# Kernel optimization log

Hardware: AMD Instinct MI355X
Metric: run time of the kernel (lower is better)

Reference implementation:

```python
import jax, jax.numpy as jnp
import numpy as np

N = 100000       # nodes
F_IN = 1433      # input features (Cora)
HID = 67         # hidden dim (hardcoded in module)
C = 7            # classes (Cora)
E = 3200000      # edges (avg degree 32)


def setup_inputs() -> dict:
    key = jax.random.key(0)
    k = jax.random.split(key, 4)
    x = jax.random.normal(k[0], (N, F_IN), dtype=jnp.float32)
    edge_index = jax.random.randint(k[1], (2, E), 0, N, dtype=jnp.int32)
    W1 = jax.random.normal(k[2], (F_IN, HID), dtype=jnp.float32) / np.float32(np.sqrt(F_IN))
    b1 = jnp.zeros((HID,), dtype=jnp.float32)
    W2 = jax.random.normal(k[3], (HID, C), dtype=jnp.float32) / np.float32(np.sqrt(HID))
    b2 = jnp.zeros((C,), dtype=jnp.float32)
    return {"x": x, "edge_index": edge_index, "W1": W1, "b1": b1, "W2": W2, "b2": b2}


def gcn_conv(x, edge_index, W, b):
    """PyG GCNConv: h = W x; out = D^-1/2 (A + I) D^-1/2 h + b."""
    n = x.shape[0]
    h = x @ W  # [n, out_dim]
    loops = jnp.arange(n, dtype=edge_index.dtype)
    row = jnp.concatenate([edge_index[0], loops])  # source
    col = jnp.concatenate([edge_index[1], loops])  # target
    deg = jax.ops.segment_sum(jnp.ones_like(col, dtype=h.dtype), col, num_segments=n)
    dinv = jnp.where(deg > 0, jax.lax.rsqrt(deg), jnp.float32(0))
    norm = dinv[row] * dinv[col]                    # [E+n]
    msg = h[row] * norm[:, None]                    # gather + scale
    out = jax.ops.segment_sum(msg, col, num_segments=n)  # scatter-add
    return out + b


def reference(x, edge_index, W1, b1, W2, b2):
    h = gcn_conv(x, edge_index, W1, b1)
    h = jax.nn.leaky_relu(h, negative_slope=0.01)
    # F.dropout(p=0.951, training=self.training) -> identity in eval mode
    h = gcn_conv(h, edge_index, W2, b2)
    return jax.nn.log_softmax(h, axis=1)
```

## Files before the change

### kernel.cpp

```cpp
#include <hip/hip_runtime.h>
#include <math.h>

#define FIN  1433
#define HID  67
#define NC   7
#define NCP  8

#define BK     32
#define KTILES 45
#define KPAD   (KTILES*BK)
#define COLP   80

typedef __attribute__((ext_vector_type(8))) short short8;
typedef __attribute__((ext_vector_type(4))) float floatx4;

static __device__ inline unsigned short f2bf(float f) {
    unsigned int u = __float_as_uint(f);
    unsigned int r = (u + 0x7fffu + ((u >> 16) & 1u)) >> 16;
    return (unsigned short)r;
}


__global__ void k_zero(int* __restrict__ cnt, int N) {
    int i = blockIdx.x * 256 + threadIdx.x;
    if (i < N) cnt[i] = 0;
}

__global__ void k_count(const int* __restrict__ dst, int* __restrict__ cnt, int E) {
    int e = blockIdx.x * 256 + threadIdx.x;
    if (e < E) atomicAdd(&cnt[dst[e]], 1);
}

__global__ void k_bsum(const int* __restrict__ cnt, int* __restrict__ bsum, int N) {
    __shared__ int s[256];
    int t = threadIdx.x;
    int i = blockIdx.x * 256 + t;
    s[t] = (i < N) ? cnt[i] : 0;
    __syncthreads();
    for (int o = 128; o > 0; o >>= 1) {
        if (t < o) s[t] += s[t + o];
        __syncthreads();
    }
    if (t == 0) bsum[blockIdx.x] = s[0];
}

__global__ void k_scanb(int* __restrict__ bsum, int nb) {
    __shared__ int s[512];
    int t = threadIdx.x;
    int v = (t < nb) ? bsum[t] : 0;
    s[t] = v;
    __syncthreads();
    for (int o = 1; o < 512; o <<= 1) {
        int tmp = (t >= o) ? s[t - o] : 0;
        __syncthreads();
        s[t] += tmp;
        __syncthreads();
    }
    if (t < nb) bsum[t] = s[t] - v;
}

__global__ void k_scan3(const int* __restrict__ cnt, const int* __restrict__ bsum,
                        int* __restrict__ rowptr, int* __restrict__ cursor,
                        float* __restrict__ dinv, int N, int E) {
    __shared__ int s[256];
    int t = threadIdx.x;
    int i = blockIdx.x * 256 + t;
    int v = (i < N) ? cnt[i] : 0;
    s[t] = v;
    __syncthreads();
    for (int o = 1; o < 256; o <<= 1) {
        int tmp = (t >= o) ? s[t - o] : 0;
        __syncthreads();
        s[t] += tmp;
        __syncthreads();
    }
    if (i < N) {
        int start = bsum[blockIdx.x] + s[t] - v;
        rowptr[i] = start;
        cursor[i] = start;
        dinv[i]   = rsqrtf((float)(v + 1));
    }
    if (i == 0) rowptr[N] = E;
}

__global__ void k_fill(const int* __restrict__ ei, int* __restrict__ cursor,
                       int* __restrict__ csrs, int E) {
    int e = blockIdx.x * 256 + threadIdx.x;
    if (e < E) {
        int s = ei[e];
        int d = ei[E + e];
        int pos = atomicAdd(&cursor[d], 1);
        csrs[pos] = s;
    }
}


__global__ void k_wcvt(const float* __restrict__ W1, const float* __restrict__ x,
                       unsigned short* __restrict__ Wt, float* __restrict__ xpad, int N) {
    int idx = blockIdx.x * 256 + threadIdx.x;
    if (idx < KPAD) xpad[idx] = (idx < FIN) ? x[(N - 1) * FIN + idx] : 0.f;
    if (idx >= COLP * KPAD) return;
    int col = idx / KPAD;
    int k   = idx - col * KPAD;
    float v = (col < HID && k < FIN) ? W1[k * HID + col] : 0.f;
    Wt[idx] = f2bf(v);
}


#define GEMM1_LOAD(Abuf, KT) __builtin_memcpy(&Abuf[0], xp0 + (KT), 32)

#define GEMM1_STEP(Abuf, KT) do {                                                   \
        short8 fa;                                                                  \
        _Pragma("unroll")                                                           \
        for (int u = 0; u < 8; u++) fa[u] = (short)f2bf(Abuf[u]);                   \
        _Pragma("unroll")                                                           \
        for (int j = 0; j < 5; j++) {                                               \
            short8 bf = *(const short8*)(wb + j * 16 * KPAD + (KT));                \
            acc[j] = __builtin_amdgcn_mfma_f32_16x16x32_bf16(fa, bf, acc[j], 0, 0, 0); \
        }                                                                           \
    } while (0)

__global__ __launch_bounds__(256) void k_gemm1(const float* __restrict__ x,
                                               const unsigned short* __restrict__ Wt,
                                               const float* __restrict__ dinv,
                                               const float* __restrict__ xpad,
                                               float* __restrict__ h64,
                                               float* __restrict__ h4, int N) {
    int t    = threadIdx.x;
    int lane = t & 63;
    int w    = t >> 6;
    int lm   = lane & 15;
    int lq   = lane >> 4;
    int row0w = blockIdx.x * 64 + w * 16;

    int r0 = row0w + lm;
    const float* xp0 = (r0 >= N - 1) ? xpad : (x + r0 * FIN);
    xp0 += lq * 8;
    const unsigned short* wb = Wt + lm * KPAD + lq * 8;

    floatx4 acc[5];
#pragma unroll
    for (int j = 0; j < 5; j++) acc[j] = (floatx4){0.f, 0.f, 0.f, 0.f};

    float A0[8], A1[8];
    GEMM1_LOAD(A0, 0);
    int kt = 0;
    for (; kt + 2 * BK < KPAD; kt += 2 * BK) {
        GEMM1_LOAD(A1, kt + BK);
        GEMM1_STEP(A0, kt);
        GEMM1_LOAD(A0, kt + 2 * BK);
        GEMM1_STEP(A1, kt + BK);
    }
    GEMM1_STEP(A0, kt);

#pragma unroll
    for (int i = 0; i < 4; i++) {
        int row = row0w + lq * 4 + i;
        if (row < N) {
            float dv = dinv[row];
            int off = row * 64;
#pragma unroll
            for (int j = 0; j < 4; j++) h64[off + j * 16 + lm] = dv * acc[j][i];
            if (lm < 4) h4[row * 4 + lm] = dv * acc[4][i];
        }
    }
}


__global__ __launch_bounds__(256) void k_agg1(const float* __restrict__ h64,
                                              const float* __restrict__ h4,
                                              const int* __restrict__ rowptr,
                                              const int* __restrict__ csrs,
                                              const float* __restrict__ dinv,
                                              const float* __restrict__ bias1,
                                              const float* __restrict__ W2,
                                              float* __restrict__ h2s, int N) {
    int lane = threadIdx.x & 63;
    int d = blockIdx.x * 4 + (threadIdx.x >> 6);
    if (d >= N) return;
    int start = rowptr[d];
    int end   = rowptr[d + 1];
    int tc = lane & 3;

    float m0 = 0.f, m1 = 0.f, m2 = 0.f, m3 = 0.f;
    float t0 = 0.f, t1 = 0.f, t2 = 0.f, t3 = 0.f;
    int e = start;
    for (; e + 4 <= end; e += 4) {
        int s0 = csrs[e], s1 = csrs[e + 1], s2 = csrs[e + 2], s3 = csrs[e + 3];
        m0 += h64[s0 * 64 + lane];  t0 += h4[s0 * 4 + tc];
        m1 += h64[s1 * 64 + lane];  t1 += h4[s1 * 4 + tc];
        m2 += h64[s2 * 64 + lane];  t2 += h4[s2 * 4 + tc];
        m3 += h64[s3 * 64 + lane];  t3 += h4[s3 * 4 + tc];
    }
    for (; e < end; e++) {
        int s = csrs[e];
        m0 += h64[s * 64 + lane];
        t0 += h4[s * 4 + tc];
    }
    float dd = dinv[d];
    float sa = ((m0 + m1) + (m2 + m3)) + h64[d * 64 + lane];
    float sb = ((t0 + t1) + (t2 + t3)) + h4[d * 4 + tc];

    float vm = bias1[lane] + dd * sa;
    vm = vm > 0.f ? vm : 0.01f * vm;
    int tcol = 64 + tc;
    float bb = (tcol < HID) ? bias1[tcol] : 0.f;
    float vt = bb + dd * sb;
    vt = vt > 0.f ? vt : 0.01f * vt;

    float pj[NC];
#pragma unroll
    for (int j = 0; j < NC; j++) {
        float wm = W2[lane * NC + j];
        float wt = (lane < 3) ? W2[(64 + lane) * NC + j] : 0.f;
        pj[j] = vm * wm + vt * wt;
    }
#pragma unroll
    for (int o = 32; o >= 1; o >>= 1) {
#pragma unroll
        for (int j = 0; j < NC; j++) pj[j] += __shfl_xor(pj[j], o);
    }
    if (lane == 0) {
        int off = d * NCP;
#pragma unroll
        for (int j = 0; j < NC; j++) h2s[off + j] = dd * pj[j];
        h2s[off + NC] = 0.f;
    }
}


__global__ __launch_bounds__(256) void k_agg2(const float* __restrict__ h2s,
                                              const int* __restrict__ rowptr,
                                              const int* __restrict__ csrs,
                                              const float* __restrict__ dinv,
                                              const float* __restrict__ b2,
                                              float* __restrict__ out, int N) {
    int lane = threadIdx.x & 63;
    int d = blockIdx.x * 4 + (threadIdx.x >> 6);
    if (d >= N) return;
    int es = lane >> 3;
    int j  = lane & 7;
    int start = rowptr[d], end = rowptr[d + 1];
    float acc = 0.f;
    for (int e = start + es; e < end; e += 8) {
        int s = csrs[e];
        acc += h2s[s * NCP + j];
    }
#pragma unroll
    for (int o = 32; o >= 8; o >>= 1) acc += __shfl_xor(acc, o);
    float dd = dinv[d];
    float self = h2s[d * NCP + j];
    float v = ((j < NC) ? b2[j] : 0.f) + dd * (self + acc);
    float mv = (j == NC) ? -1e30f : v;
#pragma unroll
    for (int o = 4; o >= 1; o >>= 1) mv = fmaxf(mv, __shfl_xor(mv, o));
    float ex = (j == NC) ? 0.f : __expf(v - mv);
    float ss = ex;
#pragma unroll
    for (int o = 4; o >= 1; o >>= 1) ss += __shfl_xor(ss, o);
    if (lane < 8 && j < NC) {
        out[d * NC + j] = v - mv - __logf(ss);
    }
}


extern "C" void kernel_launch(void* const* d_in, const int* in_sizes, int n_in,
                              void* d_out, int out_size, void* d_ws, size_t ws_size,
                              hipStream_t stream) {
    const float* x  = (const float*)d_in[0];
    const int*   ei = (const int*)d_in[1];
    const float* W1 = (const float*)d_in[2];
    const float* b1 = (const float*)d_in[3];
    const float* W2 = (const float*)d_in[4];
    const float* b2 = (const float*)d_in[5];
    float* out = (float*)d_out;

    int N = in_sizes[0] / FIN;
    int E = in_sizes[1] / 2;

    size_t o = 0;
    auto alloc = [&](size_t words) { size_t r = o; o += words; o = (o + 63) & ~(size_t)63; return r; };
    size_t o_dinv   = alloc((size_t)N);
    size_t o_cnt    = alloc((size_t)N);
    size_t o_rowptr = alloc((size_t)N + 1);
    size_t o_cursor = alloc((size_t)N);
    size_t o_bsum   = alloc(1024);
    size_t o_csrs   = alloc((size_t)E);
    size_t o_wt     = alloc((size_t)COLP * KPAD / 2);
    size_t o_xpad   = alloc((size_t)KPAD);
    size_t o_h64    = alloc((size_t)N * 64);
    size_t o_h4     = alloc((size_t)N * 4);
    size_t o_h2s    = alloc((size_t)N * NCP);

    float* wsf = (float*)d_ws;
    int*   wsi = (int*)d_ws;
    float* dinv   = wsf + o_dinv;
    int*   cnt    = wsi + o_cnt;
    int*   rowptr = wsi + o_rowptr;
    int*   cursor = wsi + o_cursor;
    int*   bsum   = wsi + o_bsum;
    int*   csrs   = wsi + o_csrs;
    unsigned short* Wt = (unsigned short*)(wsi + o_wt);
    float* xpad   = wsf + o_xpad;
    float* h64    = wsf + o_h64;
    float* h4     = wsf + o_h4;
    float* h2s    = wsf + o_h2s;

    int nb = (N + 255) / 256;
    int eb = (E + 255) / 256;
    int gb = (N + 63) / 64;

    k_zero <<<nb, 256, 0, stream>>>(cnt, N);
    k_count<<<eb, 256, 0, stream>>>(ei + E, cnt, E);
    k_bsum <<<nb, 256, 0, stream>>>(cnt, bsum, N);
    k_scanb<<<1, 512, 0, stream>>>(bsum, nb);
    k_scan3<<<nb, 256, 0, stream>>>(cnt, bsum, rowptr, cursor, dinv, N, E);
    k_fill <<<eb, 256, 0, stream>>>(ei, cursor, csrs, E);

    k_wcvt <<<(COLP * KPAD + 255) / 256, 256, 0, stream>>>(W1, x, Wt, xpad, N);
    k_gemm1<<<gb, 256, 0, stream>>>(x, Wt, dinv, xpad, h64, h4, N);
    k_agg1 <<<(N + 3) / 4, 256, 0, stream>>>(h64, h4, rowptr, csrs, dinv, b1, W2, h2s, N);
    k_agg2 <<<(N + 3) / 4, 256, 0, stream>>>(h2s, rowptr, csrs, dinv, b2, out, N);
}
```

Baseline: 1.466 ms.

## Build CSR via two-level bucket sort instead of global atomics

Replaces per-edge global atomic counting and filling of the CSR with a two-pass bucketed radix sort. Edges are first binned into 512-node coarse buckets using shared-memory histograms and block-level offsets. Each bucket is then sorted locally in LDS to produce rowptr, csrs and dinv. This cuts contended global atomics and scattered writes, at the cost of an extra E-sized buffer and packed encodings that assume node ids fit in 18 bits and at most 512 coarse buckets.

```diff
diff --git a/kernel.cpp b/kernel.cpp
--- a/kernel.cpp
+++ b/kernel.cpp
@@ -11,6 +11,9 @@
 #define KPAD   (KTILES*BK)
 #define COLP   80
 
+#define CB_BITS 9
+#define CB_SIZE 512
+
 typedef __attribute__((ext_vector_type(8))) short short8;
 typedef __attribute__((ext_vector_type(4))) float floatx4;
 
@@ -21,89 +24,138 @@
 }
 
 
-__global__ void k_zero(int* __restrict__ cnt, int N) {
-    int i = blockIdx.x * 256 + threadIdx.x;
-    if (i < N) cnt[i] = 0;
-}
-
-__global__ void k_count(const int* __restrict__ dst, int* __restrict__ cnt, int E) {
-    int e = blockIdx.x * 256 + threadIdx.x;
-    if (e < E) atomicAdd(&cnt[dst[e]], 1);
-}
-
-__global__ void k_bsum(const int* __restrict__ cnt, int* __restrict__ bsum, int N) {
-    __shared__ int s[256];
-    int t = threadIdx.x;
-    int i = blockIdx.x * 256 + t;
-    s[t] = (i < N) ? cnt[i] : 0;
-    __syncthreads();
-    for (int o = 128; o > 0; o >>= 1) {
-        if (t < o) s[t] += s[t + o];
-        __syncthreads();
-    }
-    if (t == 0) bsum[blockIdx.x] = s[0];
-}
-
-__global__ void k_scanb(int* __restrict__ bsum, int nb) {
-    __shared__ int s[512];
-    int t = threadIdx.x;
-    int v = (t < nb) ? bsum[t] : 0;
-    s[t] = v;
-    __syncthreads();
-    for (int o = 1; o < 512; o <<= 1) {
-        int tmp = (t >= o) ? s[t - o] : 0;
-        __syncthreads();
-        s[t] += tmp;
-        __syncthreads();
-    }
-    if (t < nb) bsum[t] = s[t] - v;
-}
-
-__global__ void k_scan3(const int* __restrict__ cnt, const int* __restrict__ bsum,
-                        int* __restrict__ rowptr, int* __restrict__ cursor,
-                        float* __restrict__ dinv, int N, int E) {
-    __shared__ int s[256];
-    int t = threadIdx.x;
-    int i = blockIdx.x * 256 + t;
-    int v = (i < N) ? cnt[i] : 0;
-    s[t] = v;
-    __syncthreads();
-    for (int o = 1; o < 256; o <<= 1) {
-        int tmp = (t >= o) ? s[t - o] : 0;
-        __syncthreads();
-        s[t] += tmp;
-        __syncthreads();
-    }
-    if (i < N) {
-        int start = bsum[blockIdx.x] + s[t] - v;
-        rowptr[i] = start;
-        cursor[i] = start;
-        dinv[i]   = rsqrtf((float)(v + 1));
-    }
-    if (i == 0) rowptr[N] = E;
-}
-
-__global__ void k_fill(const int* __restrict__ ei, int* __restrict__ cursor,
-                       int* __restrict__ csrs, int E) {
-    int e = blockIdx.x * 256 + threadIdx.x;
-    if (e < E) {
-        int s = ei[e];
-        int d = ei[E + e];
-        int pos = atomicAdd(&cursor[d], 1);
-        csrs[pos] = s;
-    }
-}
-
-
 __global__ void k_wcvt(const float* __restrict__ W1, const float* __restrict__ x,
-                       unsigned short* __restrict__ Wt, float* __restrict__ xpad, int N) {
+                       unsigned short* __restrict__ Wt, float* __restrict__ xpad,
+                       int* __restrict__ gcnt, int N) {
     int idx = blockIdx.x * 256 + threadIdx.x;
+    if (idx < 512) gcnt[idx] = 0;
     if (idx < KPAD) xpad[idx] = (idx < FIN) ? x[(N - 1) * FIN + idx] : 0.f;
     if (idx >= COLP * KPAD) return;
     int col = idx / KPAD;
     int k   = idx - col * KPAD;
     float v = (col < HID && k < FIN) ? W1[k * HID + col] : 0.f;
     Wt[idx] = f2bf(v);
+}
+
+
+__global__ __launch_bounds__(256) void k_cb_count(const int* __restrict__ dst,
+                                                  int* __restrict__ gcnt, int E) {
+    __shared__ int lh[512];
+    int t = threadIdx.x;
+    lh[t] = 0; lh[t + 256] = 0;
+    __syncthreads();
+    int base = blockIdx.x * 4096;
+    for (int i = t; i < 4096; i += 256) {
+        int e = base + i;
+        if (e < E) atomicAdd(&lh[dst[e] >> CB_BITS], 1);
+    }
+    __syncthreads();
+    int v0 = lh[t];       if (v0) atomicAdd(&gcnt[t], v0);
+    int v1 = lh[t + 256]; if (v1) atomicAdd(&gcnt[t + 256], v1);
+}
+
+__global__ void k_cb_scan(const int* __restrict__ gcnt, int* __restrict__ cbase,
+                          int* __restrict__ gcur, int E) {
+    __shared__ int s[512];
+    int t = threadIdx.x;
+    int v = gcnt[t];
+    s[t] = v;
+    __syncthreads();
+    for (int o = 1; o < 512; o <<= 1) {
+        int tmp = (t >= o) ? s[t - o] : 0;
+        __syncthreads();
+        s[t] += tmp;
+        __syncthreads();
+    }
+    int ex = s[t] - v;
+    cbase[t] = ex;
+    gcur[t]  = ex;
+    if (t == 511) cbase[512] = E;
+}
+
+__global__ __launch_bounds__(256) void k_cb_scat(const int* __restrict__ ei,
+                                                 int* __restrict__ gcur,
+                                                 unsigned int* __restrict__ gbuf, int E) {
+    __shared__ int lh[512];
+    __shared__ int gb[512];
+    int t = threadIdx.x;
+    lh[t] = 0; lh[t + 256] = 0;
+    __syncthreads();
+    int base = blockIdx.x * 4096;
+    unsigned int rk[16];
+    unsigned int pk[16];
+#pragma unroll
+    for (int i = 0; i < 16; i++) {
+        int e = base + i * 256 + t;
+        rk[i] = 0xFFFFFFFFu;
+        if (e < E) {
+            int s = ei[e];
+            int d = ei[E + e];
+            int cb = d >> CB_BITS;
+            int r = atomicAdd(&lh[cb], 1);
+            rk[i] = (unsigned int)((cb << 16) | r);
+            pk[i] = (unsigned int)s | ((unsigned int)(d & (CB_SIZE - 1)) << 18);
+        }
+    }
+    __syncthreads();
+    int v0 = lh[t];       gb[t]       = v0 ? atomicAdd(&gcur[t], v0) : 0;
+    int v1 = lh[t + 256]; gb[t + 256] = v1 ? atomicAdd(&gcur[t + 256], v1) : 0;
+    __syncthreads();
+#pragma unroll
+    for (int i = 0; i < 16; i++) {
+        if (rk[i] != 0xFFFFFFFFu) {
+            int cb = rk[i] >> 16, r = rk[i] & 0xFFFF;
+            gbuf[gb[cb] + r] = pk[i];
+        }
+    }
+}
+
+__global__ __launch_bounds__(256) void k_cb_build(const unsigned int* __restrict__ gbuf,
+                                                  const int* __restrict__ cbase,
+                                                  int* __restrict__ rowptr,
+                                                  int* __restrict__ csrs,
+                                                  float* __restrict__ dinv, int N, int E) {
+    __shared__ int hist[512];
+    __shared__ int sc[512];
+    int b = blockIdx.x;
+    int t = threadIdx.x;
+    int n0 = cbase[b], n1 = cbase[b + 1];
+    hist[t] = 0; hist[t + 256] = 0;
+    __syncthreads();
+    for (int i = n0 + t; i < n1; i += 256)
+        atomicAdd(&hist[gbuf[i] >> 18], 1);
+    __syncthreads();
+    sc[t] = hist[t]; sc[t + 256] = hist[t + 256];
+    __syncthreads();
+    for (int o = 1; o < 512; o <<= 1) {
+        int a0 = (t       >= o) ? sc[t - o]       : 0;
+        int a1 = (t + 256 >= o) ? sc[t + 256 - o] : 0;
+        __syncthreads();
+        sc[t] += a0; sc[t + 256] += a1;
+        __syncthreads();
+    }
+#pragma unroll
+    for (int hh = 0; hh < 2; hh++) {
+        int f = t + hh * 256;
+        int d = (b << CB_BITS) + f;
+        int cnt = hist[f];
+        int ex  = sc[f] - cnt;
+        if (d < N) {
+            rowptr[d] = n0 + ex;
+            dinv[d]   = rsqrtf((float)(cnt + 1));
+        }
+    }
+    if (b == 0 && t == 0) rowptr[N] = E;
+    __syncthreads();
+    hist[t]       = sc[t] - hist[t];
+    hist[t + 256] = sc[t + 256] - hist[t + 256];
+    __syncthreads();
+    for (int i = n0 + t; i < n1; i += 256) {
+        unsigned int pkd = gbuf[i];
+        int f = pkd >> 18;
+        int p = atomicAdd(&hist[f], 1);
+        csrs[n0 + p] = (int)(pkd & 0x3FFFFu);
+    }
 }
 
 
@@ -281,11 +333,12 @@
     size_t o = 0;
     auto alloc = [&](size_t words) { size_t r = o; o += words; o = (o + 63) & ~(size_t)63; return r; };
     size_t o_dinv   = alloc((size_t)N);
-    size_t o_cnt    = alloc((size_t)N);
     size_t o_rowptr = alloc((size_t)N + 1);
-    size_t o_cursor = alloc((size_t)N);
-    size_t o_bsum   = alloc(1024);
     size_t o_csrs   = alloc((size_t)E);
+    size_t o_gbuf   = alloc((size_t)E);
+    size_t o_gcnt   = alloc(512);
+    size_t o_cbase  = alloc(513);
+    size_t o_gcur   = alloc(512);
     size_t o_wt     = alloc((size_t)COLP * KPAD / 2);
     size_t o_xpad   = alloc((size_t)KPAD);
     size_t o_h64    = alloc((size_t)N * 64);
@@ -295,29 +348,28 @@
     float* wsf = (float*)d_ws;
     int*   wsi = (int*)d_ws;
     float* dinv   = wsf + o_dinv;
-    int*   cnt    = wsi + o_cnt;
     int*   rowptr = wsi + o_rowptr;
-    int*   cursor = wsi + o_cursor;
-    int*   bsum   = wsi + o_bsum;
     int*   csrs   = wsi + o_csrs;
+    unsigned int* gbuf = (unsigned int*)(wsi + o_gbuf);
+    int*   gcnt   = wsi + o_gcnt;
+    int*   cbase  = wsi + o_cbase;
+    int*   gcur   = wsi + o_gcur;
     unsigned short* Wt = (unsigned short*)(wsi + o_wt);
     float* xpad   = wsf + o_xpad;
     float* h64    = wsf + o_h64;
     float* h4     = wsf + o_h4;
     float* h2s    = wsf + o_h2s;
 
-    int nb = (N + 255) / 256;
-    int eb = (E + 255) / 256;
-    int gb = (N + 63) / 64;
-
-    k_zero <<<nb, 256, 0, stream>>>(cnt, N);
-    k_count<<<eb, 256, 0, stream>>>(ei + E, cnt, E);
-    k_bsum <<<nb, 256, 0, stream>>>(cnt, bsum, N);
-    k_scanb<<<1, 512, 0, stream>>>(bsum, nb);
-    k_scan3<<<nb, 256, 0, stream>>>(cnt, bsum, rowptr, cursor, dinv, N, E);
-    k_fill <<<eb, 256, 0, stream>>>(ei, cursor, csrs, E);
-
-    k_wcvt <<<(COLP * KPAD + 255) / 256, 256, 0, stream>>>(W1, x, Wt, xpad, N);
+    int eb4 = (E + 4095) / 4096;
+    int nbk = (N + CB_SIZE - 1) >> CB_BITS;
+    int gb  = (N + 63) / 64;
+
+    k_wcvt    <<<(COLP * KPAD + 255) / 256, 256, 0, stream>>>(W1, x, Wt, xpad, gcnt, N);
+    k_cb_count<<<eb4, 256, 0, stream>>>(ei + E, gcnt, E);
+    k_cb_scan <<<1, 512, 0, stream>>>(gcnt, cbase, gcur, E);
+    k_cb_scat <<<eb4, 256, 0, stream>>>(ei, gcur, gbuf, E);
+    k_cb_build<<<nbk, 256, 0, stream>>>(gbuf, cbase, rowptr, csrs, dinv, N, E);
+
     k_gemm1<<<gb, 256, 0, stream>>>(x, Wt, dinv, xpad, h64, h4, N);
     k_agg1 <<<(N + 3) / 4, 256, 0, stream>>>(h64, h4, rowptr, csrs, dinv, b1, W2, h2s, N);
     k_agg2 <<<(N + 3) / 4, 256, 0, stream>>>(h2s, rowptr, csrs, dinv, b2, out, N);
```

New measurement: 1.197 ms. 18.4% less time.
